# Optimization experiments

Hardware: AMD Instinct MI355X
Metric: run time of the kernel (lower is better)

## Reference

```python
import jax, jax.numpy as jnp
import numpy as np

N_CLASS = 32000
EMB = 256
HID = 512
NUM_LAYER = 2
BATCH = 256
SEQ = 64


def setup_inputs() -> dict:
    key = jax.random.key(0)
    ks = jax.random.split(key, 16)
    s_e = 1.0 / np.sqrt(EMB)
    s_h = 1.0 / np.sqrt(HID)
    inp = {
        "X": jax.random.randint(ks[0], (BATCH, SEQ), 0, N_CLASS, dtype=jnp.int32),
        "C": jax.random.normal(ks[1], (N_CLASS, EMB), jnp.float32),
        # torch Linear weights are [out, in]; all layers share one set (list aliasing)
        "W_ii": jax.random.uniform(ks[2], (HID, EMB), jnp.float32, -s_e, s_e),
        "W_hi": jax.random.uniform(ks[3], (HID, HID), jnp.float32, -s_h, s_h),
        "b_i": jnp.ones((HID,), jnp.float32),
        "W_if": jax.random.uniform(ks[4], (HID, EMB), jnp.float32, -s_e, s_e),
        "W_hf": jax.random.uniform(ks[5], (HID, HID), jnp.float32, -s_h, s_h),
        "b_f": jnp.ones((HID,), jnp.float32),
        "W_ig": jax.random.uniform(ks[6], (HID, EMB), jnp.float32, -s_e, s_e),
        "W_hg": jax.random.uniform(ks[7], (HID, HID), jnp.float32, -s_h, s_h),
        "b_g": jnp.ones((HID,), jnp.float32),
        "W_io": jax.random.uniform(ks[8], (HID, EMB), jnp.float32, -s_e, s_e),
        "W_ho": jax.random.uniform(ks[9], (HID, HID), jnp.float32, -s_h, s_h),
        "b_o": jnp.ones((HID,), jnp.float32),
        "W": jax.random.uniform(ks[10], (EMB, HID), jnp.float32, -s_h, s_h),
        "b": jnp.ones((EMB,), jnp.float32),
        "W_final": jax.random.uniform(ks[11], (N_CLASS, HID), jnp.float32, -s_h, s_h),
        "b_final": jnp.ones((N_CLASS,), jnp.float32),
    }
    return inp


def _lstm_forward(X, C, W_ii, W_hi, b_i, W_if, W_hf, b_f, W_ig, W_hg, b_g,
                  W_io, W_ho, b_o, W, b, W_final, b_final):
    emb = C[X]                      # [B, S, E]
    xs = jnp.swapaxes(emb, 0, 1)    # [S, B, E] (time-major)
    B = X.shape[0]
    h0 = jnp.zeros((NUM_LAYER, B, HID), jnp.float32)
    c0 = jnp.zeros((NUM_LAYER, B, HID), jnp.float32)

    def step(carry, x_t):
        h, c = carry
        x = x_t
        hs, cs = [], []
        for l in range(NUM_LAYER):  # all layers share the same weights (aliased lists)
            i = jax.nn.sigmoid(x @ W_ii.T + h[l] @ W_hi.T + b_i)
            f = jax.nn.sigmoid(x @ W_if.T + h[l] @ W_hf.T + b_f)
            g = jnp.tanh(x @ W_ig.T + h[l] @ W_hg.T + b_g)
            o = jax.nn.sigmoid(x @ W_io.T + h[l] @ W_ho.T + b_o)
            c_new = f * c[l] + i * g
            h_new = o * jnp.tanh(c_new)
            x = h_new @ W.T + b      # project back to emb_size; dropout = identity (eval)
            hs.append(h_new)
            cs.append(c_new)
        return (jnp.stack(hs), jnp.stack(cs)), None

    (h, c), _ = jax.lax.scan(step, (h0, c0), xs)
    return h[-1] @ W_final.T + b_final   # [B, n_class]


def reference(X, C, W_ii, W_hi, b_i, W_if, W_hf, b_f, W_ig, W_hg, b_g,
              W_io, W_ho, b_o, W, b, W_final, b_final):
    return _lstm_forward(X, C, W_ii, W_hi, b_i, W_if, W_hf, b_f, W_ig, W_hg, b_g,
                         W_io, W_ho, b_o, W, b, W_final, b_final)
```

## Files before the change

### kernel.cpp

```cpp
#include <hip/hip_runtime.h>
#include <hip/hip_bf16.h>
#include <math.h>

#define B 256
#define S 64
#define E 256
#define H 512
#define NC 32000

typedef __attribute__((ext_vector_type(8))) short short8;
typedef __attribute__((ext_vector_type(4))) float f32x4;

__device__ inline short f2bf(float v) {
    __hip_bfloat16 h = __float2bfloat16(v);
    return *reinterpret_cast<short*>(&h);
}
__device__ inline float bf2f(short s) {
    __hip_bfloat16 h;
    *reinterpret_cast<short*>(&h) = s;
    return __bfloat162float(h);
}

__global__ __launch_bounds__(256) void k_zero(float4* __restrict__ p, int n4) {
    int i = blockIdx.x * 256 + threadIdx.x;
    if (i < n4) p[i] = float4{0.f, 0.f, 0.f, 0.f};
}

__global__ __launch_bounds__(256) void k_trans(const float* __restrict__ W0,
                                               const float* __restrict__ W1,
                                               const float* __restrict__ W2,
                                               const float* __restrict__ W3,
                                               int K, float* __restrict__ outT) {
    __shared__ float TT[64][65];
    const int u0 = blockIdx.x * 64;
    const int k0 = blockIdx.y * 64;
    const int g  = blockIdx.z;
    const float* Wg = (g == 0) ? W0 : (g == 1) ? W1 : (g == 2) ? W2 : W3;
    const int tx = threadIdx.x & 15, ty = threadIdx.x >> 4;
#pragma unroll
    for (int i = 0; i < 4; ++i) {
        float4 v = *(const float4*)(Wg + (size_t)(u0 + ty + i * 16) * K + k0 + tx * 4);
        TT[tx * 4 + 0][ty + i * 16] = v.x;
        TT[tx * 4 + 1][ty + i * 16] = v.y;
        TT[tx * 4 + 2][ty + i * 16] = v.z;
        TT[tx * 4 + 3][ty + i * 16] = v.w;
    }
    __syncthreads();
#pragma unroll
    for (int i = 0; i < 4; ++i) {
        int kl = ty + i * 16;
        float4 o = {TT[kl][tx * 4 + 0], TT[kl][tx * 4 + 1], TT[kl][tx * 4 + 2], TT[kl][tx * 4 + 3]};
        *(float4*)(outT + (size_t)(k0 + kl) * 2048 + g * 512 + u0 + tx * 4) = o;
    }
}

__global__ __launch_bounds__(256) void k_comb(const float* __restrict__ Wi0,
                                              const float* __restrict__ Wi1,
                                              const float* __restrict__ Wi2,
                                              const float* __restrict__ Wi3,
                                              const float* __restrict__ W,
                                              float* __restrict__ WcT) {
    __shared__ float WiS[64][65];
    __shared__ float WS[64][65];
    const int g  = blockIdx.x >> 3;
    const int u0 = (blockIdx.x & 7) * 64;
    const int k0 = blockIdx.y * 64;
    const float* Wi = (g == 0) ? Wi0 : (g == 1) ? Wi1 : (g == 2) ? Wi2 : Wi3;
    const int tx = threadIdx.x & 15, ty = threadIdx.x >> 4;
    float acc[4][4] = {};
    for (int e0 = 0; e0 < E; e0 += 64) {
#pragma unroll
        for (int i = 0; i < 4; ++i) {
            float4 v = *(const float4*)(Wi + (size_t)(u0 + ty + i * 16) * E + e0 + tx * 4);
            *(float4*)&WiS[ty + i * 16][tx * 4] = v;
        }
#pragma unroll
        for (int i = 0; i < 4; ++i) {
            float4 v = *(const float4*)(W + (size_t)(e0 + ty + i * 16) * H + k0 + tx * 4);
            *(float4*)&WS[ty + i * 16][tx * 4] = v;
        }
        __syncthreads();
#pragma unroll
        for (int el = 0; el < 64; ++el) {
            float uv[4], kv[4];
#pragma unroll
            for (int j = 0; j < 4; ++j) { uv[j] = WiS[ty * 4 + j][el]; kv[j] = WS[el][tx * 4 + j]; }
#pragma unroll
            for (int i2 = 0; i2 < 4; ++i2)
#pragma unroll
                for (int j = 0; j < 4; ++j) acc[i2][j] += uv[i2] * kv[j];
        }
        __syncthreads();
    }
#pragma unroll
    for (int j = 0; j < 4; ++j) {
        float4 o = {acc[0][j], acc[1][j], acc[2][j], acc[3][j]};
        *(float4*)(WcT + (size_t)(k0 + tx * 4 + j) * 2048 + g * 512 + u0 + ty * 4) = o;
    }
}

__global__ __launch_bounds__(256) void k_bias(const float* __restrict__ WxT,
                                              const float* __restrict__ bi,
                                              const float* __restrict__ bf_,
                                              const float* __restrict__ bg_,
                                              const float* __restrict__ bo_,
                                              const float* __restrict__ bvec,
                                              float* __restrict__ bias0,
                                              float* __restrict__ bias1) {
    int c = blockIdx.x * 256 + threadIdx.x;
    int g = c >> 9, u = c & 511;
    const float* bp = (g == 0) ? bi : (g == 1) ? bf_ : (g == 2) ? bg_ : bo_;
    float basev = bp[u];
    float s = 0.f;
    for (int e = 0; e < E; ++e) s += WxT[(size_t)e * 2048 + c] * bvec[e];
    bias0[c] = basev;
    bias1[c] = basev + s;
}

__global__ __launch_bounds__(256) void k_pack(const float* __restrict__ Wt,
                                              short* __restrict__ outp) {
    int idx = blockIdx.x * 256 + threadIdx.x;
    int k = idx >> 11, n = idx & 2047;
    float v = Wt[(size_t)k * 2048 + n];
    short hi = f2bf(v);
    short lo = f2bf(v - bf2f(hi));
    int kb = k >> 5, ks = (k >> 3) & 3, j = k & 7;
    int nb = n >> 4, nl = n & 15;
    int lane = ks * 16 + nl;
    size_t base = (((size_t)kb * 128 + nb) * 2) * 512 + (size_t)lane * 8 + j;
    outp[base] = hi;
    outp[base + 512] = lo;
}

__device__ __forceinline__ void gemm_h_half(const short* __restrict__ aH,
                                            const short* __restrict__ aL,
                                            const short* __restrict__ Bp,
                                            int ubG, int lane, int ks, int khalf,
                                            f32x4 acc[4]) {
#pragma unroll 4
    for (int kb2 = 0; kb2 < 8; ++kb2) {
        int kb = khalf * 8 + kb2;
        int ko = kb * 32 + ks * 8;
        short8 ahi = *(const short8*)(aH + ko);
        short8 alo = *(const short8*)(aL + ko);
#pragma unroll
        for (int g = 0; g < 4; ++g) {
            const short* bp = Bp + ((((size_t)kb * 4 + g) * 32) + ubG) * 1024 + (size_t)lane * 8;
            short8 bhi = *(const short8*)bp;
            short8 blo = *(const short8*)(bp + 512);
            acc[g] = __builtin_amdgcn_mfma_f32_16x16x32_bf16(ahi, bhi, acc[g], 0, 0, 0);
            acc[g] = __builtin_amdgcn_mfma_f32_16x16x32_bf16(alo, bhi, acc[g], 0, 0, 0);
            acc[g] = __builtin_amdgcn_mfma_f32_16x16x32_bf16(ahi, blo, acc[g], 0, 0, 0);
        }
    }
}

__global__ __launch_bounds__(512) void k_phase(int p, const int* __restrict__ X,
        const float* __restrict__ C,
        const short* __restrict__ WxP, const short* __restrict__ WcP,
        const short* __restrict__ WhP,
        const float* __restrict__ bias0g, const float* __restrict__ bias1g,
        short* __restrict__ h0H, short* __restrict__ h0L,
        short* __restrict__ h1H, short* __restrict__ h1L,
        float* __restrict__ c0, float* __restrict__ c1) {
    const int panel = blockIdx.y;
    if (panel == 0 && p >= S) return;
    if (panel == 1 && p == 0) return;
    const int tid   = threadIdx.x;
    const int wave  = tid >> 6, lane = tid & 63;
    const int khalf = wave >> 2, wsub = wave & 3;
    const int lrow  = lane & 15, ks = lane >> 4;
    const int msup  = blockIdx.x & 3;
    const int ubG   = blockIdx.x >> 2;
    const int row   = msup * 64 + wsub * 16 + lrow;
    const int u     = ubG * 16 + lrow;

    __shared__ float red[4][64][17];

    f32x4 acc[4];
#pragma unroll
    for (int g = 0; g < 4; ++g) acc[g] = (f32x4){0.f, 0.f, 0.f, 0.f};

    if (panel == 0) {
        const int tok = X[row * S + p];
        const float* crow = C + (size_t)tok * E;
#pragma unroll
        for (int kb2 = 0; kb2 < 4; ++kb2) {
            int kb = khalf * 4 + kb2;
            int ko = kb * 32 + ks * 8;
            float4 v0 = *(const float4*)(crow + ko);
            float4 v1 = *(const float4*)(crow + ko + 4);
            float v[8] = {v0.x, v0.y, v0.z, v0.w, v1.x, v1.y, v1.z, v1.w};
            short8 ahi, alo;
#pragma unroll
            for (int j = 0; j < 8; ++j) {
                short hj = f2bf(v[j]);
                ahi[j] = hj;
                alo[j] = f2bf(v[j] - bf2f(hj));
            }
#pragma unroll
            for (int g = 0; g < 4; ++g) {
                const short* bp = WxP + ((((size_t)kb * 4 + g) * 32) + ubG) * 1024 + (size_t)lane * 8;
                short8 bhi = *(const short8*)bp;
                short8 blo = *(const short8*)(bp + 512);
                acc[g] = __builtin_amdgcn_mfma_f32_16x16x32_bf16(ahi, bhi, acc[g], 0, 0, 0);
                acc[g] = __builtin_amdgcn_mfma_f32_16x16x32_bf16(alo, bhi, acc[g], 0, 0, 0);
                acc[g] = __builtin_amdgcn_mfma_f32_16x16x32_bf16(ahi, blo, acc[g], 0, 0, 0);
            }
        }
        size_t off = (size_t)((p + 1) & 1) * B * H + (size_t)row * H;
        gemm_h_half(h0H + off, h0L + off, WhP, ubG, lane, ks, khalf, acc);
    } else {
        const int q = p - 1;
        size_t offx = (size_t)(q & 1) * B * H + (size_t)row * H;
        gemm_h_half(h0H + offx, h0L + offx, WcP, ubG, lane, ks, khalf, acc);
        size_t offh = (size_t)((q + 1) & 1) * B * H + (size_t)row * H;
        gemm_h_half(h1H + offh, h1L + offh, WhP, ubG, lane, ks, khalf, acc);
    }

    if (khalf == 1) {
#pragma unroll
        for (int g = 0; g < 4; ++g)
#pragma unroll
            for (int r = 0; r < 4; ++r) red[wsub][lane][g * 4 + r] = acc[g][r];
    }
    __syncthreads();
    if (khalf == 1) return;

#pragma unroll
    for (int g = 0; g < 4; ++g)
#pragma unroll
        for (int r = 0; r < 4; ++r) acc[g][r] += red[wsub][lane][g * 4 + r];

    short* dH; short* dL; float* cb;
    if (panel == 0) { size_t off = (size_t)(p & 1) * B * H; dH = h0H + off; dL = h0L + off; cb = c0; }
    else            { size_t off = (size_t)((p - 1) & 1) * B * H; dH = h1H + off; dL = h1L + off; cb = c1; }
    const float* bias = panel ? bias1g : bias0g;
    const float bI = bias[u], bF = bias[512 + u], bG = bias[1024 + u], bO = bias[1536 + u];
    const int rbase = msup * 64 + wsub * 16 + ks * 4;
#pragma unroll
    for (int r = 0; r < 4; ++r) {
        size_t ix = (size_t)(rbase + r) * H + u;
        float pi = acc[0][r] + bI;
        float pf = acc[1][r] + bF;
        float pg = acc[2][r] + bG;
        float po = acc[3][r] + bO;
        float iv = 1.f / (1.f + expf(-pi));
        float fv = 1.f / (1.f + expf(-pf));
        float gv = tanhf(pg);
        float ov = 1.f / (1.f + expf(-po));
        float cn = fv * cb[ix] + iv * gv;
        float hn = ov * tanhf(cn);
        cb[ix] = cn;
        short hh = f2bf(hn);
        dH[ix] = hh;
        dL[ix] = f2bf(hn - bf2f(hh));
    }
}

__global__ __launch_bounds__(1024) void k_cls(const short* __restrict__ hH,
                                              const short* __restrict__ hL,
                                              const float* __restrict__ Wf,
                                              const float* __restrict__ bfin,
                                              float* __restrict__ out) {
    const int tid  = threadIdx.x;
    const int wave = tid >> 6, lane = tid & 63;
    const int lrow = lane & 15, ks = lane >> 4;
    const int n0 = blockIdx.x * 128;
    const int m0 = wave * 16;

    __shared__ short BT[128 * 64];

    f32x4 acc[8];
#pragma unroll
    for (int nf = 0; nf < 8; ++nf) acc[nf] = (f32x4){0.f, 0.f, 0.f, 0.f};
    const short* aH = hH + (size_t)(m0 + lrow) * H;
    const short* aL = hL + (size_t)(m0 + lrow) * H;

    const int rowl = tid >> 3;
    const int kcol = (tid & 7) * 8;

    for (int kc = 0; kc < 8; ++kc) {
        {
            const float* wr = Wf + (size_t)(n0 + rowl) * H + kc * 64 + kcol;
            float4 v0 = *(const float4*)wr;
            float4 v1 = *(const float4*)(wr + 4);
            short8 bw;
            bw[0] = f2bf(v0.x); bw[1] = f2bf(v0.y); bw[2] = f2bf(v0.z); bw[3] = f2bf(v0.w);
            bw[4] = f2bf(v1.x); bw[5] = f2bf(v1.y); bw[6] = f2bf(v1.z); bw[7] = f2bf(v1.w);
            int byteoff = (rowl * 128 + kcol * 2) ^ ((rowl & 7) << 4);
            *(short8*)((char*)BT + byteoff) = bw;
        }
        __syncthreads();
#pragma unroll
        for (int kbi = 0; kbi < 2; ++kbi) {
            int ko = kc * 64 + kbi * 32 + ks * 8;
            short8 ahi = *(const short8*)(aH + ko);
            short8 alo = *(const short8*)(aL + ko);
#pragma unroll
            for (int nf = 0; nf < 8; ++nf) {
                int nl = nf * 16 + lrow;
                int byte = (nl * 128 + (kbi * 32 + ks * 8) * 2) ^ ((nl & 7) << 4);
                short8 b = *(const short8*)((const char*)BT + byte);
                acc[nf] = __builtin_amdgcn_mfma_f32_16x16x32_bf16(ahi, b, acc[nf], 0, 0, 0);
                acc[nf] = __builtin_amdgcn_mfma_f32_16x16x32_bf16(alo, b, acc[nf], 0, 0, 0);
            }
        }
        __syncthreads();
    }

#pragma unroll
    for (int nf = 0; nf < 8; ++nf) {
        int n = n0 + nf * 16 + lrow;
        float bias = bfin[n];
#pragma unroll
        for (int r = 0; r < 4; ++r) {
            int brow = m0 + ks * 4 + r;
            out[(size_t)brow * NC + n] = acc[nf][r] + bias;
        }
    }
}

extern "C" void kernel_launch(void* const* d_in, const int* in_sizes, int n_in,
                              void* d_out, int out_size, void* d_ws, size_t ws_size,
                              hipStream_t stream) {
    const int*   X    = (const int*)d_in[0];
    const float* C    = (const float*)d_in[1];
    const float* Wii  = (const float*)d_in[2];
    const float* Whi  = (const float*)d_in[3];
    const float* bi   = (const float*)d_in[4];
    const float* Wif  = (const float*)d_in[5];
    const float* Whf  = (const float*)d_in[6];
    const float* bf   = (const float*)d_in[7];
    const float* Wig  = (const float*)d_in[8];
    const float* Whg  = (const float*)d_in[9];
    const float* bg   = (const float*)d_in[10];
    const float* Wio  = (const float*)d_in[11];
    const float* Who  = (const float*)d_in[12];
    const float* bo   = (const float*)d_in[13];
    const float* W    = (const float*)d_in[14];
    const float* bvec = (const float*)d_in[15];
    const float* Wf   = (const float*)d_in[16];
    const float* bfin = (const float*)d_in[17];
    float* out = (float*)d_out;
    char* base = (char*)d_ws;

    float* WhT  = (float*)(base + 0);
    float* WxT  = (float*)(base + 4194304);
    float* WcT  = (float*)(base + 6291456);
    short* WhP  = (short*)(base + 10485760);
    short* WxP  = (short*)(base + 14680064);
    short* WcP  = (short*)(base + 16777216);
    float* bias0 = (float*)(base + 20971520);
    float* bias1 = (float*)(base + 20979712);
    short* h0H  = (short*)(base + 20987904);
    short* h0L  = (short*)(base + 21512192);
    short* h1H  = (short*)(base + 22036480);
    short* h1L  = (short*)(base + 22560768);
    float* c0   = (float*)(base + 23085056);
    float* c1   = (float*)(base + 23609344);

    k_zero<<<768, 256, 0, stream>>>((float4*)(base + 20987904), 196608);

    k_trans<<<dim3(8, 8, 4), 256, 0, stream>>>(Whi, Whf, Whg, Who, H, WhT);
    k_trans<<<dim3(8, 4, 4), 256, 0, stream>>>(Wii, Wif, Wig, Wio, E, WxT);
    k_comb<<<dim3(32, 8), 256, 0, stream>>>(Wii, Wif, Wig, Wio, W, WcT);
    k_pack<<<4096, 256, 0, stream>>>(WhT, WhP);
    k_pack<<<2048, 256, 0, stream>>>(WxT, WxP);
    k_pack<<<4096, 256, 0, stream>>>(WcT, WcP);
    k_bias<<<8, 256, 0, stream>>>(WxT, bi, bf, bg, bo, bvec, bias0, bias1);

    for (int p = 0; p <= S; ++p)
        k_phase<<<dim3(128, 2), 512, 0, stream>>>(p, X, C, WxP, WcP, WhP, bias0, bias1,
                                                  h0H, h0L, h1H, h1L, c0, c1);

    k_cls<<<250, 1024, 0, stream>>>(h1H + (size_t)B * H, h1L + (size_t)B * H, Wf, bfin, out);
}
```

Before: 1.621 ms.

## Fuse recurrent phase launches into one cooperative kernel and double-buffer classifier tiles

The 65 per-timestep k_phase launches become a single cooperative kernel, k_phases, with 256 blocks. It loops over all phases and separates them with a grid-wide sync, which removes the per-launch overhead between dependent steps. Separately, the classifier kernel now uses 64-column tiles across 500 blocks and double-buffers its shared-memory weight tile, prefetching the next K chunk during the MFMAs. The risks are the cost of grid sync itself and the requirement that all 256 blocks be co-resident.

New measurement: 6.230 ms. 284% more time.

```diff
diff --git a/kernel.cpp b/kernel.cpp
--- a/kernel.cpp
+++ b/kernel.cpp
@@ -1,6 +1,9 @@
 #include <hip/hip_runtime.h>
 #include <hip/hip_bf16.h>
+#include <hip/hip_cooperative_groups.h>
 #include <math.h>
+
+namespace cg = cooperative_groups;
 
 #define B 256
 #define S 64
@@ -9,6 +12,7 @@
 #define NC 32000
 
 typedef __attribute__((ext_vector_type(8))) short short8;
+typedef __attribute__((ext_vector_type(4))) short short4v;
 typedef __attribute__((ext_vector_type(4))) float f32x4;
 
 __device__ inline short f2bf(float v) {
@@ -155,7 +159,7 @@
     }
 }
 
-__global__ __launch_bounds__(512) void k_phase(int p, const int* __restrict__ X,
+__global__ __launch_bounds__(512) void k_phases(const int* __restrict__ X,
         const float* __restrict__ C,
         const short* __restrict__ WxP, const short* __restrict__ WcP,
         const short* __restrict__ WhP,
@@ -163,98 +167,108 @@
         short* __restrict__ h0H, short* __restrict__ h0L,
         short* __restrict__ h1H, short* __restrict__ h1L,
         float* __restrict__ c0, float* __restrict__ c1) {
-    const int panel = blockIdx.y;
-    if (panel == 0 && p >= S) return;
-    if (panel == 1 && p == 0) return;
+    cg::grid_group grid = cg::this_grid();
+
+    const int panel = blockIdx.x >> 7;
+    const int bx    = blockIdx.x & 127;
     const int tid   = threadIdx.x;
     const int wave  = tid >> 6, lane = tid & 63;
     const int khalf = wave >> 2, wsub = wave & 3;
     const int lrow  = lane & 15, ks = lane >> 4;
-    const int msup  = blockIdx.x & 3;
-    const int ubG   = blockIdx.x >> 2;
+    const int msup  = bx & 3;
+    const int ubG   = bx >> 2;
     const int row   = msup * 64 + wsub * 16 + lrow;
     const int u     = ubG * 16 + lrow;
 
     __shared__ float red[4][64][17];
 
-    f32x4 acc[4];
-#pragma unroll
-    for (int g = 0; g < 4; ++g) acc[g] = (f32x4){0.f, 0.f, 0.f, 0.f};
-
-    if (panel == 0) {
-        const int tok = X[row * S + p];
-        const float* crow = C + (size_t)tok * E;
-#pragma unroll
-        for (int kb2 = 0; kb2 < 4; ++kb2) {
-            int kb = khalf * 4 + kb2;
-            int ko = kb * 32 + ks * 8;
-            float4 v0 = *(const float4*)(crow + ko);
-            float4 v1 = *(const float4*)(crow + ko + 4);
-            float v[8] = {v0.x, v0.y, v0.z, v0.w, v1.x, v1.y, v1.z, v1.w};
-            short8 ahi, alo;
-#pragma unroll
-            for (int j = 0; j < 8; ++j) {
-                short hj = f2bf(v[j]);
-                ahi[j] = hj;
-                alo[j] = f2bf(v[j] - bf2f(hj));
-            }
-#pragma unroll
-            for (int g = 0; g < 4; ++g) {
-                const short* bp = WxP + ((((size_t)kb * 4 + g) * 32) + ubG) * 1024 + (size_t)lane * 8;
-                short8 bhi = *(const short8*)bp;
-                short8 blo = *(const short8*)(bp + 512);
-                acc[g] = __builtin_amdgcn_mfma_f32_16x16x32_bf16(ahi, bhi, acc[g], 0, 0, 0);
-                acc[g] = __builtin_amdgcn_mfma_f32_16x16x32_bf16(alo, bhi, acc[g], 0, 0, 0);
-                acc[g] = __builtin_amdgcn_mfma_f32_16x16x32_bf16(ahi, blo, acc[g], 0, 0, 0);
-            }
-        }
-        size_t off = (size_t)((p + 1) & 1) * B * H + (size_t)row * H;
-        gemm_h_half(h0H + off, h0L + off, WhP, ubG, lane, ks, khalf, acc);
-    } else {
-        const int q = p - 1;
-        size_t offx = (size_t)(q & 1) * B * H + (size_t)row * H;
-        gemm_h_half(h0H + offx, h0L + offx, WcP, ubG, lane, ks, khalf, acc);
-        size_t offh = (size_t)((q + 1) & 1) * B * H + (size_t)row * H;
-        gemm_h_half(h1H + offh, h1L + offh, WhP, ubG, lane, ks, khalf, acc);
-    }
-
-    if (khalf == 1) {
-#pragma unroll
-        for (int g = 0; g < 4; ++g)
-#pragma unroll
-            for (int r = 0; r < 4; ++r) red[wsub][lane][g * 4 + r] = acc[g][r];
-    }
-    __syncthreads();
-    if (khalf == 1) return;
-
-#pragma unroll
-    for (int g = 0; g < 4; ++g)
-#pragma unroll
-        for (int r = 0; r < 4; ++r) acc[g][r] += red[wsub][lane][g * 4 + r];
-
-    short* dH; short* dL; float* cb;
-    if (panel == 0) { size_t off = (size_t)(p & 1) * B * H; dH = h0H + off; dL = h0L + off; cb = c0; }
-    else            { size_t off = (size_t)((p - 1) & 1) * B * H; dH = h1H + off; dL = h1L + off; cb = c1; }
     const float* bias = panel ? bias1g : bias0g;
     const float bI = bias[u], bF = bias[512 + u], bG = bias[1024 + u], bO = bias[1536 + u];
+    float* cb = panel ? c1 : c0;
     const int rbase = msup * 64 + wsub * 16 + ks * 4;
-#pragma unroll
-    for (int r = 0; r < 4; ++r) {
-        size_t ix = (size_t)(rbase + r) * H + u;
-        float pi = acc[0][r] + bI;
-        float pf = acc[1][r] + bF;
-        float pg = acc[2][r] + bG;
-        float po = acc[3][r] + bO;
-        float iv = 1.f / (1.f + expf(-pi));
-        float fv = 1.f / (1.f + expf(-pf));
-        float gv = tanhf(pg);
-        float ov = 1.f / (1.f + expf(-po));
-        float cn = fv * cb[ix] + iv * gv;
-        float hn = ov * tanhf(cn);
-        cb[ix] = cn;
-        short hh = f2bf(hn);
-        dH[ix] = hh;
-        dL[ix] = f2bf(hn - bf2f(hh));
+
+    for (int p = 0; p <= S; ++p) {
+        const bool active = panel ? (p >= 1) : (p < S);
+        if (active) {
+            f32x4 acc[4];
+#pragma unroll
+            for (int g = 0; g < 4; ++g) acc[g] = (f32x4){0.f, 0.f, 0.f, 0.f};
+
+            if (panel == 0) {
+                const int tok = X[row * S + p];
+                const float* crow = C + (size_t)tok * E;
+#pragma unroll
+                for (int kb2 = 0; kb2 < 4; ++kb2) {
+                    int kb = khalf * 4 + kb2;
+                    int ko = kb * 32 + ks * 8;
+                    float4 v0 = *(const float4*)(crow + ko);
+                    float4 v1 = *(const float4*)(crow + ko + 4);
+                    float v[8] = {v0.x, v0.y, v0.z, v0.w, v1.x, v1.y, v1.z, v1.w};
+                    short8 ahi, alo;
+#pragma unroll
+                    for (int j = 0; j < 8; ++j) {
+                        short hj = f2bf(v[j]);
+                        ahi[j] = hj;
+                        alo[j] = f2bf(v[j] - bf2f(hj));
+                    }
+#pragma unroll
+                    for (int g = 0; g < 4; ++g) {
+                        const short* bp = WxP + ((((size_t)kb * 4 + g) * 32) + ubG) * 1024 + (size_t)lane * 8;
+                        short8 bhi = *(const short8*)bp;
+                        short8 blo = *(const short8*)(bp + 512);
+                        acc[g] = __builtin_amdgcn_mfma_f32_16x16x32_bf16(ahi, bhi, acc[g], 0, 0, 0);
+                        acc[g] = __builtin_amdgcn_mfma_f32_16x16x32_bf16(alo, bhi, acc[g], 0, 0, 0);
+                        acc[g] = __builtin_amdgcn_mfma_f32_16x16x32_bf16(ahi, blo, acc[g], 0, 0, 0);
+                    }
+                }
+                size_t off = (size_t)((p + 1) & 1) * B * H + (size_t)row * H;
+                gemm_h_half(h0H + off, h0L + off, WhP, ubG, lane, ks, khalf, acc);
+            } else {
+                const int q = p - 1;
+                size_t offx = (size_t)(q & 1) * B * H + (size_t)row * H;
+                gemm_h_half(h0H + offx, h0L + offx, WcP, ubG, lane, ks, khalf, acc);
+                size_t offh = (size_t)((q + 1) & 1) * B * H + (size_t)row * H;
+                gemm_h_half(h1H + offh, h1L + offh, WhP, ubG, lane, ks, khalf, acc);
+            }
+
+            if (khalf == 1) {
+#pragma unroll
+                for (int g = 0; g < 4; ++g)
+#pragma unroll
+                    for (int r = 0; r < 4; ++r) red[wsub][lane][g * 4 + r] = acc[g][r];
+            }
+            __syncthreads();
+            if (khalf == 0) {
+#pragma unroll
+                for (int g = 0; g < 4; ++g)
+#pragma unroll
+                    for (int r = 0; r < 4; ++r) acc[g][r] += red[wsub][lane][g * 4 + r];
+
+                short* dH; short* dL;
+                if (panel == 0) { size_t off = (size_t)(p & 1) * B * H; dH = h0H + off; dL = h0L + off; }
+                else            { size_t off = (size_t)((p - 1) & 1) * B * H; dH = h1H + off; dL = h1L + off; }
+#pragma unroll
+                for (int r = 0; r < 4; ++r) {
+                    size_t ix = (size_t)(rbase + r) * H + u;
+                    float pi = acc[0][r] + bI;
+                    float pf = acc[1][r] + bF;
+                    float pg = acc[2][r] + bG;
+                    float po = acc[3][r] + bO;
+                    float iv = 1.f / (1.f + expf(-pi));
+                    float fv = 1.f / (1.f + expf(-pf));
+                    float gv = tanhf(pg);
+                    float ov = 1.f / (1.f + expf(-po));
+                    float cn = fv * cb[ix] + iv * gv;
+                    float hn = ov * tanhf(cn);
+                    cb[ix] = cn;
+                    short hh = f2bf(hn);
+                    dH[ix] = hh;
+                    dL[ix] = f2bf(hn - bf2f(hh));
+                }
+            }
+        }
+        __threadfence();
+        grid.sync();
     }
 }
 
@@ -266,51 +280,54 @@
     const int tid  = threadIdx.x;
     const int wave = tid >> 6, lane = tid & 63;
     const int lrow = lane & 15, ks = lane >> 4;
-    const int n0 = blockIdx.x * 128;
+    const int n0 = blockIdx.x * 64;
     const int m0 = wave * 16;
 
-    __shared__ short BT[128 * 64];
-
-    f32x4 acc[8];
-#pragma unroll
-    for (int nf = 0; nf < 8; ++nf) acc[nf] = (f32x4){0.f, 0.f, 0.f, 0.f};
+    __shared__ short BT[2][64 * 64];
+
+    f32x4 acc[4];
+#pragma unroll
+    for (int nf = 0; nf < 4; ++nf) acc[nf] = (f32x4){0.f, 0.f, 0.f, 0.f};
     const short* aH = hH + (size_t)(m0 + lrow) * H;
     const short* aL = hL + (size_t)(m0 + lrow) * H;
 
-    const int rowl = tid >> 3;
-    const int kcol = (tid & 7) * 8;
+    const int rowl = tid >> 4;
+    const int kcol = (tid & 15) * 4;
+    const int stoff = (rowl * 128 + kcol * 2) ^ ((rowl & 7) << 4);
+    const float* wbase = Wf + (size_t)(n0 + rowl) * H + kcol;
+
+    float4 vin = *(const float4*)(wbase);
+    {
+        short4v bw = {f2bf(vin.x), f2bf(vin.y), f2bf(vin.z), f2bf(vin.w)};
+        *(short4v*)((char*)BT[0] + stoff) = bw;
+    }
+    __syncthreads();
 
     for (int kc = 0; kc < 8; ++kc) {
-        {
-            const float* wr = Wf + (size_t)(n0 + rowl) * H + kc * 64 + kcol;
-            float4 v0 = *(const float4*)wr;
-            float4 v1 = *(const float4*)(wr + 4);
-            short8 bw;
-            bw[0] = f2bf(v0.x); bw[1] = f2bf(v0.y); bw[2] = f2bf(v0.z); bw[3] = f2bf(v0.w);
-            bw[4] = f2bf(v1.x); bw[5] = f2bf(v1.y); bw[6] = f2bf(v1.z); bw[7] = f2bf(v1.w);
-            int byteoff = (rowl * 128 + kcol * 2) ^ ((rowl & 7) << 4);
-            *(short8*)((char*)BT + byteoff) = bw;
-        }
-        __syncthreads();
+        if (kc < 7) vin = *(const float4*)(wbase + (kc + 1) * 64);
 #pragma unroll
         for (int kbi = 0; kbi < 2; ++kbi) {
             int ko = kc * 64 + kbi * 32 + ks * 8;
             short8 ahi = *(const short8*)(aH + ko);
             short8 alo = *(const short8*)(aL + ko);
 #pragma unroll
-            for (int nf = 0; nf < 8; ++nf) {
+            for (int nf = 0; nf < 4; ++nf) {
                 int nl = nf * 16 + lrow;
                 int byte = (nl * 128 + (kbi * 32 + ks * 8) * 2) ^ ((nl & 7) << 4);
-                short8 b = *(const short8*)((const char*)BT + byte);
+                short8 b = *(const short8*)((const char*)BT[kc & 1] + byte);
                 acc[nf] = __builtin_amdgcn_mfma_f32_16x16x32_bf16(ahi, b, acc[nf], 0, 0, 0);
                 acc[nf] = __builtin_amdgcn_mfma_f32_16x16x32_bf16(alo, b, acc[nf], 0, 0, 0);
             }
         }
+        if (kc < 7) {
+            short4v bw = {f2bf(vin.x), f2bf(vin.y), f2bf(vin.z), f2bf(vin.w)};
+            *(short4v*)((char*)BT[(kc + 1) & 1] + stoff) = bw;
+        }
         __syncthreads();
     }
 
 #pragma unroll
-    for (int nf = 0; nf < 8; ++nf) {
+    for (int nf = 0; nf < 4; ++nf) {
         int n = n0 + nf * 16 + lrow;
         float bias = bfin[n];
 #pragma unroll
@@ -370,9 +387,14 @@
     k_pack<<<4096, 256, 0, stream>>>(WcT, WcP);
     k_bias<<<8, 256, 0, stream>>>(WxT, bi, bf, bg, bo, bvec, bias0, bias1);
 
-    for (int p = 0; p <= S; ++p)
-        k_phase<<<dim3(128, 2), 512, 0, stream>>>(p, X, C, WxP, WcP, WhP, bias0, bias1,
-                                                  h0H, h0L, h1H, h1L, c0, c1);
-
-    k_cls<<<250, 1024, 0, stream>>>(h1H + (size_t)B * H, h1L + (size_t)B * H, Wf, bfin, out);
-}
+    {
+        void* args[] = {(void*)&X, (void*)&C, (void*)&WxP, (void*)&WcP, (void*)&WhP,
+                        (void*)&bias0, (void*)&bias1,
+                        (void*)&h0H, (void*)&h0L, (void*)&h1H, (void*)&h1L,
+                        (void*)&c0, (void*)&c1};
+        hipLaunchCooperativeKernel((const void*)k_phases, dim3(256), dim3(512),
+                                   args, 0, stream);
+    }
+
+    k_cls<<<500, 1024, 0, stream>>>(h1H + (size_t)B * H, h1L + (size_t)B * H, Wf, bfin, out);
+}
```
